# Kernel tuning notes

Measured on AMD Instinct MI355X. Metric: run time of the kernel, lower is better.

The kernel has to match this reference:

```python
import jax, jax.numpy as jnp
import numpy as np

# EXP-HYDRO concrete realization of HydrologyModel.
# Parameter order matches _parameter_bounds key order; bounds per standard EXP-HYDRO.
PARAM_BOUNDS = [
    ("f",    0.0,  0.1),
    ("Smax", 100.0, 1500.0),
    ("Qmax", 10.0, 50.0),
    ("Df",   0.0,  5.0),
    ("Tmax", 0.0,  3.0),
    ("Tmin", -3.0, 0.0),
]
NEARZERO = 1e-6
T_STEPS = 1024
N_BASINS = 8192
N_PARAMS = len(PARAM_BOUNDS)


def _denormalize(static_params_norm):
    # sigmoid activation then affine map to bounds; returns dict name -> [B]
    act = jax.nn.sigmoid(static_params_norm)  # [B, P]
    return {name: lo + (hi - lo) * act[:, i]
            for i, (name, lo, hi) in enumerate(PARAM_BOUNDS)}


def _run_core(prcp, temp, pet, params, nearzero=NEARZERO):
    # prcp/temp/pet: [T, B]; params: dict of [B]
    f, Smax, Qmax = params["f"], params["Smax"], params["Qmax"]
    Df, Tmax, Tmin = params["Df"], params["Tmax"], params["Tmin"]

    def step(states, forc_t):
        snowpack, soilwater = states
        prcp_t, temp_t, pet_t = forc_t
        # hydroflux formulas (elementwise over basins)
        snowfall = jnp.where(temp_t < Tmin, prcp_t, 0.0)
        rainfall = prcp_t - snowfall
        melt = jnp.minimum(snowpack, Df * jnp.maximum(temp_t - Tmax, 0.0))
        evap = pet_t * jnp.minimum(soilwater / Smax, 1.0)
        baseflow = Qmax * jnp.exp(-f * jnp.maximum(Smax - soilwater, 0.0))
        surfaceflow = jnp.maximum(soilwater - Smax, 0.0)
        # stateflux formulas (state changes)
        d_snow = snowfall - melt
        d_soil = rainfall + melt - evap - baseflow - surfaceflow
        # state update with clamp(min=nearzero)
        new_snow = jnp.maximum(snowpack + d_snow, nearzero)
        new_soil = jnp.maximum(soilwater + d_soil, nearzero)
        out = jnp.stack([snowfall, rainfall, melt, evap,
                         baseflow, surfaceflow, d_snow, d_soil])  # [8, B]
        return (new_snow, new_soil), out

    B = prcp.shape[1]
    init = (jnp.zeros((B,), prcp.dtype), jnp.zeros((B,), prcp.dtype))
    _, outs = jax.lax.scan(step, init, (prcp, temp, pet))
    return outs  # [T, 8, B]


def setup_inputs() -> dict:
    key = jax.random.key(0)
    k1, k2, k3, k4 = jax.random.split(key, 4)
    prcp = jax.random.uniform(k1, (T_STEPS, N_BASINS), jnp.float32) * 10.0  # mm/day
    temp = jax.random.normal(k2, (T_STEPS, N_BASINS), jnp.float32) * 5.0    # deg C
    pet = jax.random.uniform(k3, (T_STEPS, N_BASINS), jnp.float32) * 5.0    # mm/day
    static_params_norm = jax.random.normal(k4, (N_BASINS, N_PARAMS), jnp.float32)
    return {"prcp": prcp, "temp": temp, "pet": pet,
            "static_params_norm": static_params_norm}


def reference(prcp, temp, pet, static_params_norm):
    params = _denormalize(static_params_norm)
    return _run_core(prcp, temp, pet, params)  # [T, 8, B]
```

## Files before the change

### kernel.cpp

```cpp
#include <hip/hip_runtime.h>
#include <stdint.h>

#define NB 8192
#define OUT_TSTRIDE (8 * NB)
#define TILE 32
#define LDS_F 6144

__device__ __forceinline__ float sigmoidf_(float x) {
    return 1.0f / (1.0f + __expf(-x));
}

__device__ __forceinline__ void async16(const float* g, float* l) {
    __builtin_amdgcn_global_load_lds(
        (const __attribute__((address_space(1))) void*)g,
        (__attribute__((address_space(3))) void*)l, 16, 0, 0);
}

__device__ __forceinline__ void fill_tile(const float* __restrict__ prcp,
                                          const float* __restrict__ temp,
                                          const float* __restrict__ pet,
                                          float* lds, int t0, int tid,
                                          int gbase) {
#pragma unroll
    for (int r = 0; r < 6; ++r) {
        const float* src = (r < 2) ? prcp : ((r < 4) ? temp : pet);
        int tt = ((r & 1) << 4) + (tid >> 4);
        int t  = t0 + tt;
        t      = (t > 1023) ? 1023 : t;
        const float* g = src + (size_t)t * NB + gbase + ((tid & 15) << 2);
        float* l       = lds + (r << 10) + (tid << 2);
        async16(g, l);
    }
}

template <int CP>
__device__ void run(const float* __restrict__ prcp,
                    const float* __restrict__ temp,
                    const float* __restrict__ pet, float* __restrict__ out,
                    float (*lds)[LDS_F], int tid, int lane, int gbase,
                    int basin, int ntiles, int lo1, int hi1, int lo2, float f,
                    float Smax, float Qmax, float Df, float Tmax, float Tmin) {
    const float rSmax = 1.0f / Smax;
    const float nf    = -f;
    float snow = 0.0f, soil = 0.0f;
    float* const outBase = out + (size_t)(2 * CP) * NB + basin;

    fill_tile(prcp, temp, pet, lds[0], 0, tid, gbase);
    __syncthreads();

    for (int tile = 0; tile < ntiles; ++tile) {
        const int cur = tile & 1;
        fill_tile(prcp, temp, pet, lds[cur ^ 1], (tile + 1) * TILE, tid, gbase);

        const bool doStore = (tile >= lo1 && tile < hi1) || (tile >= lo2);
        const float* lp    = lds[cur];
        float* o = outBase + (size_t)tile * TILE * OUT_TSTRIDE;
#pragma unroll
        for (int i = 0; i < TILE; ++i) {
            const float P  = lp[i * 64 + lane];
            const float Tm = lp[2048 + i * 64 + lane];
            const float Pe = lp[4096 + i * 64 + lane];

            const float snowfall    = (Tm < Tmin) ? P : 0.0f;
            const float rainfall    = P - snowfall;
            const float melt        = fminf(snow, Df * fmaxf(Tm - Tmax, 0.0f));
            const float evap        = Pe * fminf(soil * rSmax, 1.0f);
            const float baseflow    = Qmax * __expf(nf * fmaxf(Smax - soil, 0.0f));
            const float surfaceflow = fmaxf(soil - Smax, 0.0f);
            const float d_snow      = snowfall - melt;
            const float d_soil =
                (((rainfall + melt) - evap) - baseflow) - surfaceflow;
            snow = fmaxf(snow + d_snow, 1e-6f);
            soil = fmaxf(soil + d_soil, 1e-6f);

            if (doStore) {
                float sv0, sv1;
                if (CP == 0)      { sv0 = snowfall; sv1 = rainfall; }
                else if (CP == 1) { sv0 = melt;     sv1 = evap; }
                else if (CP == 2) { sv0 = baseflow; sv1 = surfaceflow; }
                else              { sv0 = d_snow;   sv1 = d_soil; }
                o[(size_t)i * OUT_TSTRIDE]      = sv0;
                o[(size_t)i * OUT_TSTRIDE + NB] = sv1;
            }
        }
        __syncthreads();
    }
}

extern "C" __global__ void __launch_bounds__(256, 1)
    hydro_kernel(const float* __restrict__ prcp, const float* __restrict__ temp,
                 const float* __restrict__ pet, const float* __restrict__ spn,
                 float* __restrict__ out) {
    __shared__ float lds[2][LDS_F];

    const int tid   = threadIdx.x;
    const int lane  = tid & 63;
    const int w     = tid >> 6;
    const int b     = blockIdx.x;
    const int group = (b >> 4) * 8 + (b & 7);
    const int type  = (b >> 3) & 1;
    const int gbase = group * 64;
    const int basin = gbase + lane;

    const int ntiles = type ? 24 : 32;
    const int lo1    = type ? 8 : 0;
    const int hi1    = type ? 24 : 8;
    const int lo2    = type ? 999 : 24;

    const float* p6  = spn + basin * 6;
    const float f    = 0.1f * sigmoidf_(p6[0]);
    const float Smax = 100.0f + 1400.0f * sigmoidf_(p6[1]);
    const float Qmax = 10.0f + 40.0f * sigmoidf_(p6[2]);
    const float Df   = 5.0f * sigmoidf_(p6[3]);
    const float Tmax = 3.0f * sigmoidf_(p6[4]);
    const float Tmin = -3.0f + 3.0f * sigmoidf_(p6[5]);

    switch (__builtin_amdgcn_readfirstlane(w)) {
        case 0:
            run<0>(prcp, temp, pet, out, lds, tid, lane, gbase, basin, ntiles,
                   lo1, hi1, lo2, f, Smax, Qmax, Df, Tmax, Tmin);
            break;
        case 1:
            run<1>(prcp, temp, pet, out, lds, tid, lane, gbase, basin, ntiles,
                   lo1, hi1, lo2, f, Smax, Qmax, Df, Tmax, Tmin);
            break;
        case 2:
            run<2>(prcp, temp, pet, out, lds, tid, lane, gbase, basin, ntiles,
                   lo1, hi1, lo2, f, Smax, Qmax, Df, Tmax, Tmin);
            break;
        default:
            run<3>(prcp, temp, pet, out, lds, tid, lane, gbase, basin, ntiles,
                   lo1, hi1, lo2, f, Smax, Qmax, Df, Tmax, Tmin);
            break;
    }
}

extern "C" void kernel_launch(void* const* d_in, const int* in_sizes, int n_in,
                              void* d_out, int out_size, void* d_ws,
                              size_t ws_size, hipStream_t stream) {
    const float* prcp = (const float*)d_in[0];
    const float* temp = (const float*)d_in[1];
    const float* pet  = (const float*)d_in[2];
    const float* spn  = (const float*)d_in[3];
    float* out        = (float*)d_out;

    hydro_kernel<<<dim3(256), dim3(256), 0, stream>>>(prcp, temp, pet, spn, out);
}
```

Measured before the change: 372.5 us.

## Split redundant-recurrence work across four block types with 512 blocks

```diff
diff --git a/kernel.cpp b/kernel.cpp
--- a/kernel.cpp
+++ b/kernel.cpp
@@ -38,8 +38,9 @@
                     const float* __restrict__ temp,
                     const float* __restrict__ pet, float* __restrict__ out,
                     float (*lds)[LDS_F], int tid, int lane, int gbase,
-                    int basin, int ntiles, int lo1, int hi1, int lo2, float f,
-                    float Smax, float Qmax, float Df, float Tmax, float Tmin) {
+                    int basin, int ntiles, int lo1, int hi1, int lo2, int hi2,
+                    float f, float Smax, float Qmax, float Df, float Tmax,
+                    float Tmin) {
     const float rSmax = 1.0f / Smax;
     const float nf    = -f;
     float snow = 0.0f, soil = 0.0f;
@@ -52,9 +53,10 @@
         const int cur = tile & 1;
         fill_tile(prcp, temp, pet, lds[cur ^ 1], (tile + 1) * TILE, tid, gbase);
 
-        const bool doStore = (tile >= lo1 && tile < hi1) || (tile >= lo2);
-        const float* lp    = lds[cur];
-        float* o = outBase + (size_t)tile * TILE * OUT_TSTRIDE;
+        const bool doStore =
+            (tile >= lo1 && tile < hi1) || (tile >= lo2 && tile < hi2);
+        const float* lp = lds[cur];
+        float* o        = outBase + (size_t)tile * TILE * OUT_TSTRIDE;
 #pragma unroll
         for (int i = 0; i < TILE; ++i) {
             const float P  = lp[i * 64 + lane];
@@ -87,25 +89,29 @@
     }
 }
 
-extern "C" __global__ void __launch_bounds__(256, 1)
+extern "C" __global__ void __launch_bounds__(256, 2)
     hydro_kernel(const float* __restrict__ prcp, const float* __restrict__ temp,
                  const float* __restrict__ pet, const float* __restrict__ spn,
                  float* __restrict__ out) {
     __shared__ float lds[2][LDS_F];
 
-    const int tid   = threadIdx.x;
-    const int lane  = tid & 63;
-    const int w     = tid >> 6;
-    const int b     = blockIdx.x;
-    const int group = (b >> 4) * 8 + (b & 7);
-    const int type  = (b >> 3) & 1;
+    const int tid  = threadIdx.x;
+    const int lane = tid & 63;
+    const int w    = tid >> 6;
+    const int b    = blockIdx.x;
+    const int idx  = b & 255;
+    const int pass = b >> 8;
+    const int group = (idx >> 4) * 8 + (idx & 7);
+    const int t01   = (idx >> 3) & 1;
+    const int type  = pass ? (3 - t01) : t01;
     const int gbase = group * 64;
     const int basin = gbase + lane;
 
-    const int ntiles = type ? 24 : 32;
-    const int lo1    = type ? 8 : 0;
-    const int hi1    = type ? 24 : 8;
-    const int lo2    = type ? 999 : 24;
+    const int ntiles = (8 - type) * 4;
+    const int lo1    = type * 4;
+    const int hi1    = lo1 + 4;
+    const int lo2    = (7 - type) * 4;
+    const int hi2    = lo2 + 4;
 
     const float* p6  = spn + basin * 6;
     const float f    = 0.1f * sigmoidf_(p6[0]);
@@ -118,19 +124,19 @@
     switch (__builtin_amdgcn_readfirstlane(w)) {
         case 0:
             run<0>(prcp, temp, pet, out, lds, tid, lane, gbase, basin, ntiles,
-                   lo1, hi1, lo2, f, Smax, Qmax, Df, Tmax, Tmin);
+                   lo1, hi1, lo2, hi2, f, Smax, Qmax, Df, Tmax, Tmin);
             break;
         case 1:
             run<1>(prcp, temp, pet, out, lds, tid, lane, gbase, basin, ntiles,
-                   lo1, hi1, lo2, f, Smax, Qmax, Df, Tmax, Tmin);
+                   lo1, hi1, lo2, hi2, f, Smax, Qmax, Df, Tmax, Tmin);
             break;
         case 2:
             run<2>(prcp, temp, pet, out, lds, tid, lane, gbase, basin, ntiles,
-                   lo1, hi1, lo2, f, Smax, Qmax, Df, Tmax, Tmin);
+                   lo1, hi1, lo2, hi2, f, Smax, Qmax, Df, Tmax, Tmin);
             break;
         default:
             run<3>(prcp, temp, pet, out, lds, tid, lane, gbase, basin, ntiles,
-                   lo1, hi1, lo2, f, Smax, Qmax, Df, Tmax, Tmin);
+                   lo1, hi1, lo2, hi2, f, Smax, Qmax, Df, Tmax, Tmin);
             break;
     }
 }
@@ -144,5 +150,5 @@
     const float* spn  = (const float*)d_in[3];
     float* out        = (float*)d_out;
 
-    hydro_kernel<<<dim3(256), dim3(256), 0, stream>>>(prcp, temp, pet, spn, out);
+    hydro_kernel<<<dim3(512), dim3(256), 0, stream>>>(prcp, temp, pet, spn, out);
 }
```

After: 368.6 us. No clear change (-1.1%).
